# Kernel tuning notes

Measured on AMD Instinct MI355X. Metric: run time of the kernel, lower is better.

Reference implementation:

```python
import jax, jax.numpy as jnp
import numpy as np

# config mirroring init_kwargs
PPD = (64, 64)                      # points_per_dim (spatial grid)
GRID_RANGE = ((-1.0, 1.0), (-1.0, 1.0))
B, N, NT, DX, DZ = 2, 2048, 8, 3, 16
INIT_LS = 0.1
TIME_DIM = 0


def construct_grid():
    axes = [jnp.linspace(lo, hi, p, dtype=jnp.float32) for (lo, hi), p in zip(GRID_RANGE, PPD)]
    mesh = jnp.meshgrid(*axes, indexing='ij')
    return jnp.stack(mesh, axis=-1)  # (H, W, 2)


def setup_inputs() -> dict:
    key = jax.random.key(0)
    k1, k2, k3 = jax.random.split(key, 3)
    x = jax.random.uniform(k1, (B, N, DX), jnp.float32, -1.0, 1.0)
    z = jax.random.normal(k2, (B, N, DZ), jnp.float32)
    time_grid = jnp.sort(jax.random.uniform(k3, (B, NT), jnp.float32, -1.0, 1.0), axis=-1)
    # raw parameter s.t. softplus(param) == INIT_LS (inverse-softplus init)
    lengthscale_param = jnp.full((DX,), float(np.log(np.exp(INIT_LS) - 1.0)), jnp.float32)
    return {"x": x, "z": z, "time_grid": time_grid, "lengthscale_param": lengthscale_param}


def reference(x, z, time_grid, lengthscale_param):
    H, W = PPD
    b = x.shape[0]
    t = time_grid.shape[1]
    grid = construct_grid()  # (H, W, 2)

    ls = 1e-5 + jax.nn.softplus(lengthscale_param)  # (DX,)

    # x_grid: [b, t, H, W, DX] with the time coordinate at coord index TIME_DIM(=0)
    spatial = jnp.broadcast_to(grid, (b, t, H, W, 2))
    tg = jnp.broadcast_to(time_grid[:, :, None, None, None], (b, t, H, W, 1))
    x_grid = jnp.concatenate([tg, spatial], axis=-1)

    G = t * H * W
    xg_flat = x_grid.reshape(b, G, DX)

    # pre_exp[b, g, n] = sum_d (xg - x)^2 / ls_d^2, computed via scaled-coordinate
    # norm expansion to avoid materializing the [b, G, n, DX] difference tensor.
    a = xg_flat / ls                          # [b, G, DX]
    c = x / ls                                # [b, n, DX]
    pre_exp = (jnp.sum(a * a, axis=-1)[:, :, None]
               + jnp.sum(c * c, axis=-1)[:, None, :]
               - 2.0 * jnp.einsum('bgd,bnd->bgn', a, c))
    weights = jnp.exp(-0.5 * pre_exp)         # [b, G, n]  (RBF weights)

    z_grid = jnp.einsum('bgn,bne->bge', weights, z)  # [b, G, DZ]
    z_grid = z_grid.reshape(b, t, H, W, DZ)
    return x_grid, z_grid
```

## Files before the change

### kernel.cpp

```cpp
#include <hip/hip_runtime.h>
#include <math.h>

#define B_  2
#define N_  2048
#define NT_ 8
#define DZ_ 16
#define H_  64
#define W_  64

#define XGRID_SIZE (B_*NT_*H_*W_*3)
#define CUT 12.0f
#define CH  128

using half8   = __attribute__((ext_vector_type(8))) _Float16;
using floatx4 = __attribute__((ext_vector_type(4))) float;

__global__ __launch_bounds__(256, 4) void fused_kernel(
    const float* __restrict__ x,
    const float* __restrict__ z,
    const float* __restrict__ tg,
    const float* __restrict__ lsp,
    float* __restrict__ out)
{
    const int i    = blockIdx.x & 63;
    const int t    = (blockIdx.x >> 6) & 7;
    const int b    = blockIdx.x >> 9;
    const int tid  = threadIdx.x;
    const int w    = tid >> 6;
    const int lane = tid & 63;
    const int quad = lane >> 4;
    const int col  = lane & 15;

    const float step = 2.0f / 63.0f;
    const float C    = 0.84932180f;

    const float r0 = C / (1e-5f + log1pf(expf(lsp[0])));
    const float r1 = C / (1e-5f + log1pf(expf(lsp[1])));
    const float r2 = C / (1e-5f + log1pf(expf(lsp[2])));

    const float tval = tg[b*NT_ + t];
    const float gi   = -1.0f + step * (float)i;

    union REDU {
        float2 cuc[N_ + CH];
        float  red[4][64][DZ_ + 1];
    };
    __shared__ REDU sm;
    __shared__ int  cidx[N_ + CH];
    __shared__ int  s_cnt;

    if (tid == 0) s_cnt = 0;
    __syncthreads();

    const float* __restrict__ xb = x + b*N_*3;
    {
        float px0[8], px1[8], px2[8];
        #pragma unroll
        for (int r = 0; r < 8; ++r) {
            int k = r*256 + tid;
            px0[r] = xb[k*3 + 0];
            px1[r] = xb[k*3 + 1];
            px2[r] = xb[k*3 + 2];
        }
        #pragma unroll
        for (int r = 0; r < 8; ++r) {
            int k = r*256 + tid;
            float dt = (tval - px0[r]) * r0;
            float di = (gi   - px1[r]) * r1;
            float sq = fmaf(dt, dt, di*di);
            bool keep = (sq < CUT);
            unsigned long long mb = __ballot(keep);
            int cnt = __popcll(mb);
            int base = 0;
            if (lane == 0) base = atomicAdd(&s_cnt, cnt);
            base = __shfl(base, 0, 64);
            if (keep) {
                int rank = __popcll(mb & ((1ull << lane) - 1ull));
                int pos  = base + rank;
                sm.cuc[pos] = make_float2(sq, px2[r] * r2);
                cidx[pos]   = k;
            }
        }
    }

    if (tid < 192) {
        int jj = tid / 3;
        int c  = tid - jj*3;
        float gj = -1.0f + step * (float)jj;
        float v  = (c == 0) ? tval : ((c == 1) ? gi : gj);
        out[(size_t)blockIdx.x * 192 + tid] = v;
    }

    __syncthreads();
    const int M = s_cnt;
    if (tid < CH) {
        sm.cuc[M + tid] = make_float2(1e9f, 0.f);
        cidx[M + tid]   = 0;
    }
    __syncthreads();

    const int NC = (M + CH - 1) / CH;

    const float* __restrict__ zb = z + b*N_*DZ_;
    const int koff = w*32 + (quad << 3);

    const float aj0 = (-1.0f + step * (float)( 0 + col)) * r2;
    const float aj1 = (-1.0f + step * (float)(16 + col)) * r2;
    const float aj2 = (-1.0f + step * (float)(32 + col)) * r2;
    const float aj3 = (-1.0f + step * (float)(48 + col)) * r2;

    floatx4 acc0 = {0.f,0.f,0.f,0.f};
    floatx4 acc1 = {0.f,0.f,0.f,0.f};
    floatx4 acc2 = {0.f,0.f,0.f,0.f};
    floatx4 acc3 = {0.f,0.f,0.f,0.f};

    float zreg[8];
    {
        int idx[8];
        #pragma unroll
        for (int jj = 0; jj < 8; ++jj) idx[jj] = cidx[koff + jj];
        #pragma unroll
        for (int jj = 0; jj < 8; ++jj)
            zreg[jj] = zb[(size_t)idx[jj] * DZ_ + col];
    }

    for (int c = 0; c < NC; ++c) {
        half8 bf;
        #pragma unroll
        for (int jj = 0; jj < 8; ++jj) bf[jj] = (_Float16)zreg[jj];

        const int base = c*CH + koff;
        float2 mm[8];
        #pragma unroll
        for (int jj = 0; jj < 8; ++jj) mm[jj] = sm.cuc[base + jj];

        if (c + 1 < NC) {
            const int base2 = (c + 1)*CH + koff;
            int idx[8];
            #pragma unroll
            for (int jj = 0; jj < 8; ++jj) idx[jj] = cidx[base2 + jj];
            #pragma unroll
            for (int jj = 0; jj < 8; ++jj)
                zreg[jj] = zb[(size_t)idx[jj] * DZ_ + col];
        }

        half8 a0, a1, a2, a3;
        #pragma unroll
        for (int jj = 0; jj < 8; ++jj) {
            float s  = mm[jj].x;
            float cx = mm[jj].y;
            float d0 = aj0 - cx;
            float d1 = aj1 - cx;
            float d2 = aj2 - cx;
            float d3 = aj3 - cx;
            a0[jj] = (_Float16)exp2f(-fmaf(d0, d0, s));
            a1[jj] = (_Float16)exp2f(-fmaf(d1, d1, s));
            a2[jj] = (_Float16)exp2f(-fmaf(d2, d2, s));
            a3[jj] = (_Float16)exp2f(-fmaf(d3, d3, s));
        }

        acc0 = __builtin_amdgcn_mfma_f32_16x16x32_f16(a0, bf, acc0, 0, 0, 0);
        acc1 = __builtin_amdgcn_mfma_f32_16x16x32_f16(a1, bf, acc1, 0, 0, 0);
        acc2 = __builtin_amdgcn_mfma_f32_16x16x32_f16(a2, bf, acc2, 0, 0, 0);
        acc3 = __builtin_amdgcn_mfma_f32_16x16x32_f16(a3, bf, acc3, 0, 0, 0);
    }

    __syncthreads();

    #pragma unroll
    for (int r = 0; r < 4; ++r) sm.red[w][ 0 + quad*4 + r][col] = acc0[r];
    #pragma unroll
    for (int r = 0; r < 4; ++r) sm.red[w][16 + quad*4 + r][col] = acc1[r];
    #pragma unroll
    for (int r = 0; r < 4; ++r) sm.red[w][32 + quad*4 + r][col] = acc2[r];
    #pragma unroll
    for (int r = 0; r < 4; ++r) sm.red[w][48 + quad*4 + r][col] = acc3[r];
    __syncthreads();

    const int jj = tid >> 2;
    const int eg = (tid & 3) * 4;
    float4 s4 = make_float4(0.f, 0.f, 0.f, 0.f);
    #pragma unroll
    for (int ww = 0; ww < 4; ++ww) {
        s4.x += sm.red[ww][jj][eg + 0];
        s4.y += sm.red[ww][jj][eg + 1];
        s4.z += sm.red[ww][jj][eg + 2];
        s4.w += sm.red[ww][jj][eg + 3];
    }
    float* og = out + XGRID_SIZE + (size_t)blockIdx.x * (W_ * DZ_);
    *(float4*)(og + jj*DZ_ + eg) = s4;
}

extern "C" void kernel_launch(void* const* d_in, const int* in_sizes, int n_in,
                              void* d_out, int out_size, void* d_ws, size_t ws_size,
                              hipStream_t stream) {
    const float* x   = (const float*)d_in[0];
    const float* z   = (const float*)d_in[1];
    const float* tg  = (const float*)d_in[2];
    const float* lsp = (const float*)d_in[3];

    float* out = (float*)d_out;

    fused_kernel<<<1024, 256, 0, stream>>>(x, z, tg, lsp, out);
}
```

Baseline: 71.91 us.

## Bin cutoff candidates per 16-column j-tile so each wave handles its own tile

Each surviving point is now assigned to the 16-wide j-tiles its third-coordinate radius can reach, and each wave processes only its own tile's candidate list. Previously every wave computed weights for all 64 columns over a shared list. The change also drops the cross-wave LDS reduction, packs the z index into a float4 metadata entry, and double-buffers the prefetch of metadata and z gathers. The goal is to skip exp and MFMA work for points far from a tile. It adds four ballot/atomic passes per point, and the per-tile lists are capped at LMAX, so points past the cap are silently dropped.

```diff
diff --git a/kernel.cpp b/kernel.cpp
--- a/kernel.cpp
+++ b/kernel.cpp
@@ -9,11 +9,44 @@
 #define W_  64
 
 #define XGRID_SIZE (B_*NT_*H_*W_*3)
-#define CUT 12.0f
-#define CH  128
+#define CUT  12.0f
+#define LCAP 384
+#define LMAX (LCAP - 64)
 
 using half8   = __attribute__((ext_vector_type(8))) _Float16;
 using floatx4 = __attribute__((ext_vector_type(4))) float;
+
+#if __has_builtin(__builtin_amdgcn_exp2f)
+#define EXP2(xx) __builtin_amdgcn_exp2f(xx)
+#else
+#define EXP2(xx) exp2f(xx)
+#endif
+
+
+#define STEP(mC, zC, mN, zN, KS)                                          \
+  {                                                                       \
+    const int  nxt = (KS) + 1;                                            \
+    const bool pf  = (nxt < NK2);                                         \
+    if (pf) {                                                             \
+      const int nb = (nxt << 5) + kq;                                     \
+      _Pragma("unroll")                                                   \
+      for (int jj = 0; jj < 8; ++jj) mN[jj] = mw[nb + jj];                \
+    }                                                                     \
+    half8 bf, af;                                                         \
+    _Pragma("unroll")                                                     \
+    for (int jj = 0; jj < 8; ++jj) bf[jj] = (_Float16)zC[jj];             \
+    _Pragma("unroll")                                                     \
+    for (int jj = 0; jj < 8; ++jj) {                                      \
+      float d = ajv - mC[jj].y;                                           \
+      af[jj] = (_Float16)EXP2(-fmaf(d, d, mC[jj].x));                     \
+    }                                                                     \
+    if (pf) {                                                             \
+      _Pragma("unroll")                                                   \
+      for (int jj = 0; jj < 8; ++jj)                                      \
+        zN[jj] = zb[(size_t)__float_as_int(mN[jj].z) * DZ_ + col];        \
+    }                                                                     \
+    acc = __builtin_amdgcn_mfma_f32_16x16x32_f16(af, bf, acc, 0, 0, 0);   \
+  }
 
 __global__ __launch_bounds__(256, 4) void fused_kernel(
     const float* __restrict__ x,
@@ -31,25 +64,22 @@
     const int quad = lane >> 4;
     const int col  = lane & 15;
 
-    const float step = 2.0f / 63.0f;
-    const float C    = 0.84932180f;
+    const float step    = 2.0f / 63.0f;
+    const float invstep = 31.5f;
+    const float C       = 0.84932180f;
 
     const float r0 = C / (1e-5f + log1pf(expf(lsp[0])));
     const float r1 = C / (1e-5f + log1pf(expf(lsp[1])));
     const float r2 = C / (1e-5f + log1pf(expf(lsp[2])));
+    const float RADJ = 3.74165739f / r2;
 
     const float tval = tg[b*NT_ + t];
     const float gi   = -1.0f + step * (float)i;
 
-    union REDU {
-        float2 cuc[N_ + CH];
-        float  red[4][64][DZ_ + 1];
-    };
-    __shared__ REDU sm;
-    __shared__ int  cidx[N_ + CH];
-    __shared__ int  s_cnt;
+    __shared__ float4 meta[4][LCAP];
+    __shared__ int    cnt[4];
 
-    if (tid == 0) s_cnt = 0;
+    if (tid < 4) cnt[tid] = 0;
     __syncthreads();
 
     const float* __restrict__ xb = x + b*N_*3;
@@ -69,16 +99,25 @@
             float di = (gi   - px1[r]) * r1;
             float sq = fmaf(dt, dt, di*di);
             bool keep = (sq < CUT);
-            unsigned long long mb = __ballot(keep);
-            int cnt = __popcll(mb);
-            int base = 0;
-            if (lane == 0) base = atomicAdd(&s_cnt, cnt);
-            base = __shfl(base, 0, 64);
-            if (keep) {
-                int rank = __popcll(mb & ((1ull << lane) - 1ull));
-                int pos  = base + rank;
-                sm.cuc[pos] = make_float2(sq, px2[r] * r2);
-                cidx[pos]   = k;
+            float xr = px2[r];
+            int jlo = (int)ceilf ((xr - RADJ + 1.0f) * invstep) - 1;
+            int jhi = (int)floorf((xr + RADJ + 1.0f) * invstep) + 1;
+            jlo = jlo < 0  ? 0  : jlo;
+            jhi = jhi > 63 ? 63 : jhi;
+            const int tlo = jlo >> 4, thi = jhi >> 4;
+            const float4 val = make_float4(sq, xr * r2, __int_as_float(k), 0.f);
+            #pragma unroll
+            for (int tt = 0; tt < 4; ++tt) {
+                bool kt = keep && (tt >= tlo) && (tt <= thi);
+                unsigned long long mb = __ballot(kt);
+                int cb = __popcll(mb);
+                int base = 0;
+                if (lane == 0 && cb) base = atomicAdd(&cnt[tt], cb);
+                base = __shfl(base, 0, 64);
+                if (kt) {
+                    int pos = base + __popcll(mb & ((1ull << lane) - 1ull));
+                    if (pos < LMAX) meta[tt][pos] = val;
+                }
             }
         }
     }
@@ -92,103 +131,40 @@
     }
 
     __syncthreads();
-    const int M = s_cnt;
-    if (tid < CH) {
-        sm.cuc[M + tid] = make_float2(1e9f, 0.f);
-        cidx[M + tid]   = 0;
+    {
+        int tt = tid >> 6, o = tid & 63;
+        int Lt = min(cnt[tt], LMAX);
+        meta[tt][Lt + o] = make_float4(1e9f, 0.f, __int_as_float(0), 0.f);
     }
     __syncthreads();
 
-    const int NC = (M + CH - 1) / CH;
+    const float* __restrict__ zb = z + b*N_*DZ_;
+    const float4* mw = &meta[w][0];
+    const int kq  = quad << 3;
+    const int Lw  = min(cnt[w], LMAX);
+    const int NK2 = (((Lw + 31) >> 5) + 1) & ~1;
 
-    const float* __restrict__ zb = z + b*N_*DZ_;
-    const int koff = w*32 + (quad << 3);
+    const float ajv = (-1.0f + step * (float)((w << 4) + col)) * r2;
 
-    const float aj0 = (-1.0f + step * (float)( 0 + col)) * r2;
-    const float aj1 = (-1.0f + step * (float)(16 + col)) * r2;
-    const float aj2 = (-1.0f + step * (float)(32 + col)) * r2;
-    const float aj3 = (-1.0f + step * (float)(48 + col)) * r2;
+    floatx4 acc = {0.f, 0.f, 0.f, 0.f};
+    float4 mA[8], mB[8];
+    float  zA[8], zB[8];
 
-    floatx4 acc0 = {0.f,0.f,0.f,0.f};
-    floatx4 acc1 = {0.f,0.f,0.f,0.f};
-    floatx4 acc2 = {0.f,0.f,0.f,0.f};
-    floatx4 acc3 = {0.f,0.f,0.f,0.f};
+    #pragma unroll
+    for (int jj = 0; jj < 8; ++jj) mA[jj] = mw[kq + jj];
+    #pragma unroll
+    for (int jj = 0; jj < 8; ++jj)
+        zA[jj] = zb[(size_t)__float_as_int(mA[jj].z) * DZ_ + col];
 
-    float zreg[8];
-    {
-        int idx[8];
-        #pragma unroll
-        for (int jj = 0; jj < 8; ++jj) idx[jj] = cidx[koff + jj];
-        #pragma unroll
-        for (int jj = 0; jj < 8; ++jj)
-            zreg[jj] = zb[(size_t)idx[jj] * DZ_ + col];
+    for (int ks = 0; ks < NK2; ks += 2) {
+        STEP(mA, zA, mB, zB, ks);
+        STEP(mB, zB, mA, zA, ks + 1);
     }
 
-    for (int c = 0; c < NC; ++c) {
-        half8 bf;
-        #pragma unroll
-        for (int jj = 0; jj < 8; ++jj) bf[jj] = (_Float16)zreg[jj];
-
-        const int base = c*CH + koff;
-        float2 mm[8];
-        #pragma unroll
-        for (int jj = 0; jj < 8; ++jj) mm[jj] = sm.cuc[base + jj];
-
-        if (c + 1 < NC) {
-            const int base2 = (c + 1)*CH + koff;
-            int idx[8];
-            #pragma unroll
-            for (int jj = 0; jj < 8; ++jj) idx[jj] = cidx[base2 + jj];
-            #pragma unroll
-            for (int jj = 0; jj < 8; ++jj)
-                zreg[jj] = zb[(size_t)idx[jj] * DZ_ + col];
-        }
-
-        half8 a0, a1, a2, a3;
-        #pragma unroll
-        for (int jj = 0; jj < 8; ++jj) {
-            float s  = mm[jj].x;
-            float cx = mm[jj].y;
-            float d0 = aj0 - cx;
-            float d1 = aj1 - cx;
-            float d2 = aj2 - cx;
-            float d3 = aj3 - cx;
-            a0[jj] = (_Float16)exp2f(-fmaf(d0, d0, s));
-            a1[jj] = (_Float16)exp2f(-fmaf(d1, d1, s));
-            a2[jj] = (_Float16)exp2f(-fmaf(d2, d2, s));
-            a3[jj] = (_Float16)exp2f(-fmaf(d3, d3, s));
-        }
-
-        acc0 = __builtin_amdgcn_mfma_f32_16x16x32_f16(a0, bf, acc0, 0, 0, 0);
-        acc1 = __builtin_amdgcn_mfma_f32_16x16x32_f16(a1, bf, acc1, 0, 0, 0);
-        acc2 = __builtin_amdgcn_mfma_f32_16x16x32_f16(a2, bf, acc2, 0, 0, 0);
-        acc3 = __builtin_amdgcn_mfma_f32_16x16x32_f16(a3, bf, acc3, 0, 0, 0);
-    }
-
-    __syncthreads();
-
+    float* og = out + XGRID_SIZE + (size_t)blockIdx.x * (W_ * DZ_);
     #pragma unroll
-    for (int r = 0; r < 4; ++r) sm.red[w][ 0 + quad*4 + r][col] = acc0[r];
-    #pragma unroll
-    for (int r = 0; r < 4; ++r) sm.red[w][16 + quad*4 + r][col] = acc1[r];
-    #pragma unroll
-    for (int r = 0; r < 4; ++r) sm.red[w][32 + quad*4 + r][col] = acc2[r];
-    #pragma unroll
-    for (int r = 0; r < 4; ++r) sm.red[w][48 + quad*4 + r][col] = acc3[r];
-    __syncthreads();
-
-    const int jj = tid >> 2;
-    const int eg = (tid & 3) * 4;
-    float4 s4 = make_float4(0.f, 0.f, 0.f, 0.f);
-    #pragma unroll
-    for (int ww = 0; ww < 4; ++ww) {
-        s4.x += sm.red[ww][jj][eg + 0];
-        s4.y += sm.red[ww][jj][eg + 1];
-        s4.z += sm.red[ww][jj][eg + 2];
-        s4.w += sm.red[ww][jj][eg + 3];
-    }
-    float* og = out + XGRID_SIZE + (size_t)blockIdx.x * (W_ * DZ_);
-    *(float4*)(og + jj*DZ_ + eg) = s4;
+    for (int r = 0; r < 4; ++r)
+        og[((w << 4) + (quad << 2) + r) * DZ_ + col] = acc[r];
 }
 
 extern "C" void kernel_launch(void* const* d_in, const int* in_sizes, int n_in,
```

Result: slower. 76.24 us (+6.0%).

## Replace atomic stream compaction with ballot prefix-scan and use raw exp2 builtin

Applied to the files above, without the earlier changes.

The candidate compaction stage now has each thread load 8 contiguous points with vectorized float4 loads and compute a per-thread keep mask. A bit-sliced ballot prefix sum plus a per-wave total in shared memory gives write offsets, replacing the per-iteration shared atomicAdd and shuffle. This also drops one barrier and the s_cnt initialization. The exp2 in the MFMA loop switches to the raw hardware builtin to skip denormal and range handling. Candidate order changes from strided to contiguous, which alters gather patterns on z and could affect the order of the fp16 accumulation.

```diff
diff --git a/kernel.cpp b/kernel.cpp
--- a/kernel.cpp
+++ b/kernel.cpp
@@ -14,6 +14,12 @@
 
 using half8   = __attribute__((ext_vector_type(8))) _Float16;
 using floatx4 = __attribute__((ext_vector_type(4))) float;
+
+#if __has_builtin(__builtin_amdgcn_exp2f)
+#define EXP2(xx) __builtin_amdgcn_exp2f(xx)
+#else
+#define EXP2(xx) exp2f(xx)
+#endif
 
 __global__ __launch_bounds__(256, 4) void fused_kernel(
     const float* __restrict__ x,
@@ -47,40 +53,61 @@
     };
     __shared__ REDU sm;
     __shared__ int  cidx[N_ + CH];
-    __shared__ int  s_cnt;
-
-    if (tid == 0) s_cnt = 0;
-    __syncthreads();
+    __shared__ int  wsum[4];
 
     const float* __restrict__ xb = x + b*N_*3;
+    float sq[8], cx[8];
+    int keepm = 0;
     {
-        float px0[8], px1[8], px2[8];
+        const float4* __restrict__ xb4 = (const float4*)xb;
+        float f[24];
+        #pragma unroll
+        for (int q = 0; q < 6; ++q) {
+            float4 v = xb4[tid*6 + q];
+            f[q*4+0] = v.x; f[q*4+1] = v.y; f[q*4+2] = v.z; f[q*4+3] = v.w;
+        }
         #pragma unroll
         for (int r = 0; r < 8; ++r) {
-            int k = r*256 + tid;
-            px0[r] = xb[k*3 + 0];
-            px1[r] = xb[k*3 + 1];
-            px2[r] = xb[k*3 + 2];
-        }
+            float dt = (tval - f[3*r+0]) * r0;
+            float di = (gi   - f[3*r+1]) * r1;
+            sq[r] = fmaf(dt, dt, di*di);
+            cx[r] = f[3*r+2] * r2;
+            if (sq[r] < CUT) keepm |= (1 << r);
+        }
+    }
+    const int cnt = __popc(keepm);
+    const unsigned long long below = (1ull << lane) - 1ull;
+    int pre = 0, wtot = 0;
+    #pragma unroll
+    for (int bit = 0; bit < 4; ++bit) {
+        unsigned long long bb = __ballot((cnt >> bit) & 1);
+        pre  += __popcll(bb & below) << bit;
+        wtot += __popcll(bb) << bit;
+    }
+    if (lane == 0) wsum[w] = wtot;
+    __syncthreads();
+
+    int woff = 0, M = 0;
+    #pragma unroll
+    for (int ww = 0; ww < 4; ++ww) {
+        int s = wsum[ww];
+        woff += (ww < w) ? s : 0;
+        M    += s;
+    }
+    {
+        int pos = woff + pre;
         #pragma unroll
         for (int r = 0; r < 8; ++r) {
-            int k = r*256 + tid;
-            float dt = (tval - px0[r]) * r0;
-            float di = (gi   - px1[r]) * r1;
-            float sq = fmaf(dt, dt, di*di);
-            bool keep = (sq < CUT);
-            unsigned long long mb = __ballot(keep);
-            int cnt = __popcll(mb);
-            int base = 0;
-            if (lane == 0) base = atomicAdd(&s_cnt, cnt);
-            base = __shfl(base, 0, 64);
-            if (keep) {
-                int rank = __popcll(mb & ((1ull << lane) - 1ull));
-                int pos  = base + rank;
-                sm.cuc[pos] = make_float2(sq, px2[r] * r2);
-                cidx[pos]   = k;
+            if ((keepm >> r) & 1) {
+                sm.cuc[pos] = make_float2(sq[r], cx[r]);
+                cidx[pos]   = tid*8 + r;
+                ++pos;
             }
         }
+    }
+    if (tid < CH) {
+        sm.cuc[M + tid] = make_float2(1e9f, 0.f);
+        cidx[M + tid]   = 0;
     }
 
     if (tid < 192) {
@@ -89,13 +116,6 @@
         float gj = -1.0f + step * (float)jj;
         float v  = (c == 0) ? tval : ((c == 1) ? gi : gj);
         out[(size_t)blockIdx.x * 192 + tid] = v;
-    }
-
-    __syncthreads();
-    const int M = s_cnt;
-    if (tid < CH) {
-        sm.cuc[M + tid] = make_float2(1e9f, 0.f);
-        cidx[M + tid]   = 0;
     }
     __syncthreads();
 
@@ -148,15 +168,15 @@
         #pragma unroll
         for (int jj = 0; jj < 8; ++jj) {
             float s  = mm[jj].x;
-            float cx = mm[jj].y;
-            float d0 = aj0 - cx;
-            float d1 = aj1 - cx;
-            float d2 = aj2 - cx;
-            float d3 = aj3 - cx;
-            a0[jj] = (_Float16)exp2f(-fmaf(d0, d0, s));
-            a1[jj] = (_Float16)exp2f(-fmaf(d1, d1, s));
-            a2[jj] = (_Float16)exp2f(-fmaf(d2, d2, s));
-            a3[jj] = (_Float16)exp2f(-fmaf(d3, d3, s));
+            float cxv = mm[jj].y;
+            float d0 = aj0 - cxv;
+            float d1 = aj1 - cxv;
+            float d2 = aj2 - cxv;
+            float d3 = aj3 - cxv;
+            a0[jj] = (_Float16)EXP2(-fmaf(d0, d0, s));
+            a1[jj] = (_Float16)EXP2(-fmaf(d1, d1, s));
+            a2[jj] = (_Float16)EXP2(-fmaf(d2, d2, s));
+            a3[jj] = (_Float16)EXP2(-fmaf(d3, d3, s));
         }
 
         acc0 = __builtin_amdgcn_mfma_f32_16x16x32_f16(a0, bf, acc0, 0, 0, 0);
```

Result: faster. 69.55 us (-3.3%).
